# Kernel tuning notes

Measured on AMD Instinct MI355X. Metric: run time of the kernel, lower is better.

## Reference

```python
import math
import jax, jax.numpy as jnp
import numpy as np

PROB_SPARSE_FACTOR = 0.4


def setup_inputs() -> dict:
    key = jax.random.key(0)
    kq, kk, kv = jax.random.split(key, 3)
    B, H, T, S, D = 2, 16, 2048, 2048, 64
    q = jax.random.normal(kq, (B, H, T, D), dtype=jnp.float32)
    k = jax.random.normal(kk, (B, H, S, D), dtype=jnp.float32)
    v = jax.random.normal(kv, (B, H, S, D), dtype=jnp.float32)
    return {"q": q, "k": k, "v": v}


def reference(q, k, v):
    B, H, T, D = q.shape
    S = k.shape[2]
    scaling = 1.0 / math.sqrt(D)
    # Informer-style top-u query count (static, derived from shapes)
    u = max(int(min(PROB_SPARSE_FACTOR * math.log(S), T * 0.5)), int(T * 0.3))

    # KLD scoring over full attention approximation: [B,H,T,S]
    attn_approx = jnp.einsum("bhtd,bhsd->bhts", q * scaling, k)
    attn_approx = jnp.clip(attn_approx, -50.0, 50.0)
    attn_approx = attn_approx - jnp.max(attn_approx, axis=-1, keepdims=True)
    sm = jax.nn.softmax(attn_approx, axis=-1)
    log_uniform = math.log(S)
    kl_score = jnp.sum(sm * (jnp.log(sm + 1e-10) + log_uniform), axis=-1)  # [B,H,T]

    # Select top-u most informative queries per (b,h)
    _, topk_idx = jax.lax.top_k(kl_score, u)  # [B,H,u]

    # Sparse attention only for selected queries
    q_red = jnp.take_along_axis(q, topk_idx[..., None], axis=2)  # [B,H,u,D]
    scores = jnp.einsum("bhud,bhsd->bhus", q_red, k) * scaling
    scores = jnp.clip(scores, -50.0, 50.0)
    scores = scores - jnp.max(scores, axis=-1, keepdims=True)
    w = jax.nn.softmax(scores, axis=-1)
    w = jnp.clip(w, 1e-9, 1.0)
    out_red = jnp.einsum("bhus,bhsd->bhud", w, v)  # [B,H,u,D]

    # Scatter reduced outputs back into a zero-initialized full output
    b_i = jnp.arange(B)[:, None, None]
    h_i = jnp.arange(H)[None, :, None]
    out = jnp.zeros_like(q).at[b_i, h_i, topk_idx].set(out_red)
    return out
```

## Files before the change

### kernel.cpp

```cpp
#include <hip/hip_runtime.h>
#include <math.h>

#define T_DIM 2048
#define S_DIM 2048
#define D_DIM 64
#define BH_DIM 32
#define U_SEL 614
#define LOG_S_D 7.624618986159398
#define LOG2E_F 1.4426950408889634f
#define LN2_D 0.6931471805599453
#define SCL_Q (0.125f * LOG2E_F)

typedef __attribute__((ext_vector_type(8))) short bf16x8;
typedef __attribute__((ext_vector_type(4))) short bf16x4;
typedef __attribute__((ext_vector_type(4))) float f32x4;

__device__ __forceinline__ unsigned short bf16_rne(float x) {
  unsigned u = __float_as_uint(x);
  u += 0x7FFF + ((u >> 16) & 1);
  return (unsigned short)(u >> 16);
}
__device__ __forceinline__ float bf16_to_f(unsigned short h) {
  return __uint_as_float(((unsigned)h) << 16);
}

#define GLD_LDS16(g, l)                                                        \
  __builtin_amdgcn_global_load_lds(                                            \
      (const __attribute__((address_space(1))) unsigned int*)(const void*)(g), \
      (__attribute__((address_space(3))) unsigned int*)(void*)(l), 16, 0, 0)

__device__ __forceinline__ void stage_img16(const unsigned short* __restrict__ g,
                                            unsigned short* l, int lane, int w) {
#pragma unroll
  for (int it = 0; it < 4; ++it) {
    const int chunk = it * 4 + w;
    GLD_LDS16((const char*)g + chunk * 1024 + lane * 16, (char*)l + chunk * 1024);
  }
}
__device__ __forceinline__ void stage_img8(const unsigned short* __restrict__ g,
                                           unsigned short* l, int lane, int w) {
#pragma unroll
  for (int it = 0; it < 2; ++it) {
    const int chunk = it * 4 + w;
    GLD_LDS16((const char*)g + chunk * 1024 + lane * 16, (char*)l + chunk * 1024);
  }
}

__device__ __forceinline__ bf16x8 ldfrag_sw(const unsigned short* buf, int row, int chunk) {
  return *(const bf16x8*)(buf + (row << 6) + (((chunk) ^ (row & 7)) << 3));
}
__device__ __forceinline__ bf16x8 ldfrag_k128(const unsigned short* buf, int row, int chunk) {
  return *(const bf16x8*)(buf + ((row >> 6) << 12) + ((row & 63) << 6) +
                          (((chunk) ^ (row & 7)) << 3));
}

__global__ __launch_bounds__(256) void convert_kernel(
    const float* __restrict__ kin, const float* __restrict__ vin,
    unsigned short* __restrict__ kimg, unsigned short* __restrict__ vt_g,
    float* __restrict__ out) {
  __shared__ float vld[128][65];
  const int jb = blockIdx.x;
  const int tid = threadIdx.x;
  if (jb < 1024) {
    const int bh = jb >> 5, tl = jb & 31;
    const float* src = kin + ((size_t)bh * 2048 + tl * 64) * 64;
    unsigned short* dst = kimg + (size_t)(bh * 32 + tl) * 8192;
#pragma unroll
    for (int g = 0; g < 2; ++g) {
      const int flat = g * 256 + tid;
      const int r = flat >> 3, c = flat & 7;
      const float4 f0 = *(const float4*)(src + r * 64 + c * 8);
      const float4 f1 = *(const float4*)(src + r * 64 + c * 8 + 4);
      const float xs[8] = {f0.x, f0.y, f0.z, f0.w, f1.x, f1.y, f1.z, f1.w};
      bf16x8 hv, lv;
#pragma unroll
      for (int j = 0; j < 8; ++j) {
        const unsigned short h = bf16_rne(xs[j]);
        hv[j] = (short)h;
        lv[j] = (short)bf16_rne(xs[j] - bf16_to_f(h));
      }
      const int base = (r << 6) + ((c ^ (r & 7)) << 3);
      *(bf16x8*)(dst + base) = hv;
      *(bf16x8*)(dst + 4096 + base) = lv;
    }
  } else if (jb < 1536) {
    const int jv = jb - 1024;
    const int bh = jv >> 4, tl = jv & 15;
    const float* src = vin + ((size_t)bh * 2048 + tl * 128) * 64;
#pragma unroll
    for (int g = 0; g < 8; ++g) {
      const int f = g * 256 + tid;
      const int r = f >> 4, c4 = f & 15;
      const float4 x = *(const float4*)(src + r * 64 + c4 * 4);
      vld[r][c4 * 4 + 0] = x.x;
      vld[r][c4 * 4 + 1] = x.y;
      vld[r][c4 * 4 + 2] = x.z;
      vld[r][c4 * 4 + 3] = x.w;
    }
    __syncthreads();
    unsigned short* dst = vt_g + (size_t)(bh * 16 + tl) * 8192;
#pragma unroll
    for (int g = 0; g < 4; ++g) {
      const int oc = g * 256 + tid;
      const int d = oc >> 4, cc = oc & 15;
      bf16x8 hv;
#pragma unroll
      for (int j = 0; j < 8; ++j) hv[j] = (short)bf16_rne(vld[cc * 8 + j][d]);
      *(bf16x8*)(dst + (d << 7) + (((cc ^ (d & 15))) << 3)) = hv;
    }
  } else {
    float4* o4 = (float4*)out;
    const size_t b = (size_t)(jb - 1536);
#pragma unroll
    for (int g = 0; g < 8; ++g)
      o4[b * 2048 + g * 256 + tid] = make_float4(0.f, 0.f, 0.f, 0.f);
  }
}

__global__ __launch_bounds__(256, 4) void kl_score_mfma(
    const float* __restrict__ q, const unsigned short* __restrict__ kimg,
    float2* __restrict__ zw) {
  __shared__ __align__(16) unsigned short lbuf[2][8192];
  const int b = blockIdx.x;
  const int bh = b & 31;
  const int t0 = ((b >> 5) & 15) * 128;
  const int shalf = b >> 9;
  const int tid = threadIdx.x;
  const int lane = tid & 63, w = tid >> 6, quad = lane >> 4, l15 = lane & 15;
  const float* qb = q + (size_t)bh * (2048 * 64) + (size_t)t0 * 64;
  const unsigned short* kb = kimg + (size_t)bh * (32 * 8192);
  const int tg0 = shalf * 16;

  {
#pragma unroll
    for (int g = 0; g < 4; ++g) {
      const int flat = g * 256 + tid;
      const int r = flat >> 3, c = flat & 7;
      const float4 f0 = *(const float4*)(qb + r * 64 + c * 8);
      const float4 f1 = *(const float4*)(qb + r * 64 + c * 8 + 4);
      const float xs[8] = {f0.x, f0.y, f0.z, f0.w, f1.x, f1.y, f1.z, f1.w};
      bf16x8 hv, lv;
#pragma unroll
      for (int j = 0; j < 8; ++j) {
        const float x = xs[j] * SCL_Q;
        const unsigned short h = bf16_rne(x);
        hv[j] = (short)h;
        lv[j] = (short)bf16_rne(x - bf16_to_f(h));
      }
      const int r2 = r & 63, hi2 = r >> 6;
      const int base = hi2 * 4096 + (r2 << 6) + ((c ^ (r2 & 7)) << 3);
      *(bf16x8*)(&lbuf[0][0] + base) = hv;
      *(bf16x8*)(&lbuf[1][0] + base) = lv;
    }
  }
  __syncthreads();

  bf16x8 ah[2][2], al[2][2];
#pragma unroll
  for (int rt = 0; rt < 2; ++rt) {
    const int row = w * 32 + rt * 16 + l15;
#pragma unroll
    for (int kc = 0; kc < 2; ++kc) {
      ah[rt][kc] = ldfrag_k128(&lbuf[0][0], row, kc * 4 + quad);
      al[rt][kc] = ldfrag_k128(&lbuf[1][0], row, kc * 4 + quad);
    }
  }
  __syncthreads();

  stage_img16(kb + (size_t)tg0 * 8192, &lbuf[0][0], lane, w);
  __syncthreads();

  float Zf[8], Wf[8];
#pragma unroll
  for (int i = 0; i < 8; ++i) { Zf[i] = 0.f; Wf[i] = 0.f; }

  for (int t = 0; t < 16; ++t) {
    if (t < 15)
      stage_img16(kb + (size_t)(tg0 + t + 1) * 8192, &lbuf[(t + 1) & 1][0], lane, w);
    const unsigned short* cb = &lbuf[t & 1][0];

    f32x4 acc[2][4];
#pragma unroll
    for (int rt = 0; rt < 2; ++rt)
#pragma unroll
      for (int ct = 0; ct < 4; ++ct) acc[rt][ct] = (f32x4){0.f, 0.f, 0.f, 0.f};

#pragma unroll
    for (int ct = 0; ct < 4; ++ct) {
      const int srow = ct * 16 + l15;
      const bf16x8 bh0 = ldfrag_sw(cb, srow, quad);
      const bf16x8 bl0 = ldfrag_sw(cb + 4096, srow, quad);
      const bf16x8 bh1 = ldfrag_sw(cb, srow, 4 + quad);
      const bf16x8 bl1 = ldfrag_sw(cb + 4096, srow, 4 + quad);
#pragma unroll
      for (int rt = 0; rt < 2; ++rt) {
        f32x4 c = acc[rt][ct];
        c = __builtin_amdgcn_mfma_f32_16x16x32_bf16(ah[rt][0], bh0, c, 0, 0, 0);
        c = __builtin_amdgcn_mfma_f32_16x16x32_bf16(al[rt][0], bh0, c, 0, 0, 0);
        c = __builtin_amdgcn_mfma_f32_16x16x32_bf16(ah[rt][0], bl0, c, 0, 0, 0);
        c = __builtin_amdgcn_mfma_f32_16x16x32_bf16(ah[rt][1], bh1, c, 0, 0, 0);
        c = __builtin_amdgcn_mfma_f32_16x16x32_bf16(al[rt][1], bh1, c, 0, 0, 0);
        c = __builtin_amdgcn_mfma_f32_16x16x32_bf16(ah[rt][1], bl1, c, 0, 0, 0);
        acc[rt][ct] = c;
      }
    }

#pragma unroll
    for (int rt = 0; rt < 2; ++rt)
#pragma unroll
      for (int r = 0; r < 4; ++r) {
        float zp = 0.f, wp = 0.f;
#pragma unroll
        for (int ct = 0; ct < 4; ++ct) {
          const float tt = acc[rt][ct][r];
          const float e = exp2f(tt);
          zp += e;
          wp = fmaf(e, tt, wp);
        }
        Zf[rt * 4 + r] += zp;
        Wf[rt * 4 + r] += wp;
      }
    __syncthreads();
  }

#pragma unroll
  for (int i = 0; i < 8; ++i) {
    float Zt = Zf[i], Wt = Wf[i];
#pragma unroll
    for (int mask = 1; mask <= 8; mask <<= 1) {
      Zt += __shfl_xor(Zt, mask);
      Wt += __shfl_xor(Wt, mask);
    }
    if (l15 == 0) {
      const int row = t0 + w * 32 + (i >> 2) * 16 + quad * 4 + (i & 3);
      zw[((size_t)shalf * 32 + bh) * 2048 + row] = make_float2(Zt, Wt);
    }
  }
}

__global__ __launch_bounds__(1024) void topk_kernel(const float2* __restrict__ zw,
                                                    int* __restrict__ topk) {
  __shared__ float sv[2048];
  __shared__ int si[2048];
  const int bh = blockIdx.x;
  const int tid = threadIdx.x;
  for (int i = tid; i < 2048; i += 1024) {
    const float2 a = zw[(size_t)bh * 2048 + i];
    const float2 c = zw[(size_t)(32 + bh) * 2048 + i];
    const double Z = (double)a.x + (double)c.x;
    const double W = (double)a.y + (double)c.y;
    sv[i] = (float)(LN2_D * (W / Z) - log(Z) + LOG_S_D);
    si[i] = i;
  }
  __syncthreads();
  for (int kk = 2; kk <= 2048; kk <<= 1) {
    for (int j = kk >> 1; j > 0; j >>= 1) {
      const int p = tid;
      const int i = ((p & ~(j - 1)) << 1) | (p & (j - 1));
      const int pr = i | j;
      const float v1 = sv[i], v2 = sv[pr];
      const int i1 = si[i], i2 = si[pr];
      const bool beforePI = (v2 > v1) || (v2 == v1 && i2 < i1);
      const bool dirDesc = ((i & kk) == 0);
      const bool doSwap = dirDesc ? beforePI : !beforePI;
      if (doSwap) { sv[i] = v2; sv[pr] = v1; si[i] = i2; si[pr] = i1; }
      __syncthreads();
    }
  }
  for (int i = tid; i < U_SEL; i += 1024) topk[bh * U_SEL + i] = si[i];
}

struct __align__(16) SmC {
  unsigned short qs[64 * 64];
  unsigned short kt[128 * 64];
  union { unsigned short vt[64 * 128]; float obuf[64 * 64]; } u;
  unsigned short ps[4][64 * 40];
  float zred[4][64];
};

__global__ __launch_bounds__(256, 3) void sparse_attn_mfma(
    const float* __restrict__ q, const unsigned short* __restrict__ kimg,
    const unsigned short* __restrict__ vt_g, const int* __restrict__ topk,
    float* __restrict__ out) {
  __shared__ SmC sm;
  const int b = blockIdx.x;
  const int bh = b & 31;
  const int l0 = (b >> 5) * 64;
  const int tid = threadIdx.x;
  const int lane = tid & 63, w = tid >> 6, quad = lane >> 4, l15 = lane & 15;
  const float* qb = q + (size_t)bh * (2048 * 64);
  const unsigned short* kb = kimg + (size_t)bh * (32 * 8192);
  const unsigned short* vtb = vt_g + (size_t)bh * (16 * 8192);
  const int* tkb = topk + bh * U_SEL;

  {
#pragma unroll
    for (int g = 0; g < 2; ++g) {
      const int ch = g * 256 + tid;
      const int r = ch >> 3, c = ch & 7;
      const int l = l0 + r;
      const int row = (l < U_SEL) ? tkb[l] : tkb[0];
      const float4 f0 = *(const float4*)(qb + (size_t)row * 64 + c * 8);
      const float4 f1 = *(const float4*)(qb + (size_t)row * 64 + c * 8 + 4);
      const float xs[8] = {f0.x, f0.y, f0.z, f0.w, f1.x, f1.y, f1.z, f1.w};
      bf16x8 hv;
#pragma unroll
      for (int j = 0; j < 8; ++j) hv[j] = (short)bf16_rne(xs[j] * SCL_Q);
      *(bf16x8*)&sm.qs[(r << 6) + ((c ^ (r & 7)) << 3)] = hv;
    }
  }
  stage_img8(kb, sm.kt, lane, w);
  stage_img8(kb + 8192, sm.kt + 4096, lane, w);
  stage_img16(vtb, sm.u.vt, lane, w);
  __syncthreads();

  bf16x8 qf[4][2];
#pragma unroll
  for (int nt = 0; nt < 4; ++nt)
#pragma unroll
    for (int kc = 0; kc < 2; ++kc)
      qf[nt][kc] = ldfrag_sw(sm.qs, nt * 16 + l15, kc * 4 + quad);

  float zrun[4] = {0.f, 0.f, 0.f, 0.f};
  f32x4 oacc[4][4];
#pragma unroll
  for (int a = 0; a < 4; ++a)
#pragma unroll
    for (int b2 = 0; b2 < 4; ++b2) oacc[a][b2] = (f32x4){0.f, 0.f, 0.f, 0.f};

  for (int st = 0; st < 16; ++st) {
    f32x4 sacc[2][4];
#pragma unroll
    for (int mt = 0; mt < 2; ++mt)
#pragma unroll
      for (int nt = 0; nt < 4; ++nt) sacc[mt][nt] = (f32x4){0.f, 0.f, 0.f, 0.f};
#pragma unroll
    for (int mt = 0; mt < 2; ++mt) {
      const int arow = w * 32 + mt * 16 + l15;
      const bf16x8 a0 = ldfrag_k128(sm.kt, arow, quad);
      const bf16x8 a1 = ldfrag_k128(sm.kt, arow, 4 + quad);
#pragma unroll
      for (int nt = 0; nt < 4; ++nt) {
        f32x4 c = sacc[mt][nt];
        c = __builtin_amdgcn_mfma_f32_16x16x32_bf16(a0, qf[nt][0], c, 0, 0, 0);
        c = __builtin_amdgcn_mfma_f32_16x16x32_bf16(a1, qf[nt][1], c, 0, 0, 0);
        sacc[mt][nt] = c;
      }
    }

#pragma unroll
    for (int nt = 0; nt < 4; ++nt) {
      float zl = 0.f;
#pragma unroll
      for (int mt = 0; mt < 2; ++mt) {
        bf16x4 pw;
#pragma unroll
        for (int r = 0; r < 4; ++r) {
          const float p = exp2f(sacc[mt][nt][r]);
          zl += p;
          pw[r] = (short)bf16_rne(p);
        }
        *(bf16x4*)&sm.ps[w][(nt * 16 + l15) * 40 + mt * 16 + quad * 4] = pw;
      }
      zrun[nt] += zl;
    }

    {
      bf16x8 vbf[4];
#pragma unroll
      for (int dt = 0; dt < 4; ++dt) {
        const int d = dt * 16 + l15;
        vbf[dt] = *(const bf16x8*)&sm.u.vt[(d << 7) + (((w * 4 + quad) ^ l15) << 3)];
      }
#pragma unroll
      for (int mtq = 0; mtq < 4; ++mtq) {
        const bf16x8 pa = *(const bf16x8*)&sm.ps[w][(mtq * 16 + l15) * 40 + quad * 8];
#pragma unroll
        for (int dt = 0; dt < 4; ++dt)
          oacc[mtq][dt] = __builtin_amdgcn_mfma_f32_16x16x32_bf16(pa, vbf[dt], oacc[mtq][dt], 0, 0, 0);
      }
    }
    __syncthreads();
    if (st < 15) {
      stage_img8(kb + (size_t)(2 * st + 2) * 8192, sm.kt, lane, w);
      stage_img8(kb + (size_t)(2 * st + 3) * 8192, sm.kt + 4096, lane, w);
      stage_img16(vtb + (size_t)(st + 1) * 8192, sm.u.vt, lane, w);
      __syncthreads();
    }
  }

#pragma unroll
  for (int nt = 0; nt < 4; ++nt) {
    float z = zrun[nt];
    z += __shfl_xor(z, 16);
    z += __shfl_xor(z, 32);
    if (quad == 0) sm.zred[w][nt * 16 + l15] = z;
  }
  for (int i = tid; i < 64 * 64; i += 256) sm.u.obuf[i] = 0.f;
  __syncthreads();
#pragma unroll
  for (int mtq = 0; mtq < 4; ++mtq)
#pragma unroll
    for (int r = 0; r < 4; ++r) {
      const int qr = mtq * 16 + quad * 4 + r;
#pragma unroll
      for (int dt = 0; dt < 4; ++dt)
        atomicAdd(&sm.u.obuf[qr * 64 + dt * 16 + l15], oacc[mtq][dt][r]);
    }
  __syncthreads();
  {
    const int qr = tid >> 2, seg = tid & 3;
    const int l = l0 + qr;
    if (l < U_SEL) {
      const float Zt = sm.zred[0][qr] + sm.zred[1][qr] + sm.zred[2][qr] + sm.zred[3][qr];
      const float inv = 1.0f / Zt;
      const int row = tkb[l];
      float* op = &out[((size_t)bh * T_DIM + row) * 64 + seg * 16];
      const float* ob = &sm.u.obuf[qr * 64 + seg * 16];
#pragma unroll
      for (int j = 0; j < 4; ++j) {
        float4 o;
        o.x = ob[j * 4 + 0] * inv;
        o.y = ob[j * 4 + 1] * inv;
        o.z = ob[j * 4 + 2] * inv;
        o.w = ob[j * 4 + 3] * inv;
        *(float4*)&op[j * 4] = o;
      }
    }
  }
}

extern "C" void kernel_launch(void* const* d_in, const int* in_sizes, int n_in,
                              void* d_out, int out_size, void* d_ws, size_t ws_size,
                              hipStream_t stream) {
  const float* q = (const float*)d_in[0];
  const float* k = (const float*)d_in[1];
  const float* v = (const float*)d_in[2];
  float* out = (float*)d_out;
  char* ws = (char*)d_ws;
  float2* zw = (float2*)ws;
  int* topk = (int*)(ws + 1048576);
  unsigned short* kimg = (unsigned short*)(ws + 1310720);
  unsigned short* vt_g = (unsigned short*)(ws + 18087936);

  convert_kernel<<<dim3(2048), dim3(256), 0, stream>>>(k, v, kimg, vt_g, out);
  kl_score_mfma<<<dim3(1024), dim3(256), 0, stream>>>(q, kimg, zw);
  topk_kernel<<<dim3(BH_DIM), dim3(1024), 0, stream>>>(zw, topk);
  sparse_attn_mfma<<<dim3(320), dim3(256), 0, stream>>>(q, kimg, vt_g, topk, out);
}
```

Measured before the change: 250.2 us.

## Double-buffer K tiles and register-prefetch V to overlap loads with MFMA

K tiles now use two shared-memory buffers, and the next step's K is staged into the idle buffer at the start of each iteration. The next V tile is loaded into registers early and written to shared memory after the barrier. The goal is to hide global-memory latency behind the QK and PV MFMA work instead of stalling after each step. The price is more LDS and registers, so launch bounds drop from 3 to 2 blocks per CU, which cuts occupancy.

```diff
diff --git a/kernel.cpp b/kernel.cpp
--- a/kernel.cpp
+++ b/kernel.cpp
@@ -272,13 +272,13 @@
 
 struct __align__(16) SmC {
   unsigned short qs[64 * 64];
-  unsigned short kt[128 * 64];
-  union { unsigned short vt[64 * 128]; float obuf[64 * 64]; } u;
+  union { unsigned short kt[2][128 * 64]; float obuf[64 * 64]; } u;
+  unsigned short vt[64 * 128];
   unsigned short ps[4][64 * 40];
   float zred[4][64];
 };
 
-__global__ __launch_bounds__(256, 3) void sparse_attn_mfma(
+__global__ __launch_bounds__(256, 2) void sparse_attn_mfma(
     const float* __restrict__ q, const unsigned short* __restrict__ kimg,
     const unsigned short* __restrict__ vt_g, const int* __restrict__ topk,
     float* __restrict__ out) {
@@ -309,9 +309,9 @@
       *(bf16x8*)&sm.qs[(r << 6) + ((c ^ (r & 7)) << 3)] = hv;
     }
   }
-  stage_img8(kb, sm.kt, lane, w);
-  stage_img8(kb + 8192, sm.kt + 4096, lane, w);
-  stage_img16(vtb, sm.u.vt, lane, w);
+  stage_img8(kb, sm.u.kt[0], lane, w);
+  stage_img8(kb + 8192, sm.u.kt[0] + 4096, lane, w);
+  stage_img16(vtb, sm.vt, lane, w);
   __syncthreads();
 
   bf16x8 qf[4][2];
@@ -329,6 +329,19 @@
     for (int b2 = 0; b2 < 4; ++b2) oacc[a][b2] = (f32x4){0.f, 0.f, 0.f, 0.f};
 
   for (int st = 0; st < 16; ++st) {
+    uint4 vr0, vr1, vr2, vr3;
+    if (st < 15) {
+      unsigned short* kdst = sm.u.kt[(st + 1) & 1];
+      stage_img8(kb + (size_t)(2 * st + 2) * 8192, kdst, lane, w);
+      stage_img8(kb + (size_t)(2 * st + 3) * 8192, kdst + 4096, lane, w);
+      const char* vsrc = (const char*)(vtb + (size_t)(st + 1) * 8192) + tid * 16;
+      vr0 = *(const uint4*)(vsrc);
+      vr1 = *(const uint4*)(vsrc + 4096);
+      vr2 = *(const uint4*)(vsrc + 8192);
+      vr3 = *(const uint4*)(vsrc + 12288);
+    }
+    const unsigned short* kcur = sm.u.kt[st & 1];
+
     f32x4 sacc[2][4];
 #pragma unroll
     for (int mt = 0; mt < 2; ++mt)
@@ -337,8 +350,8 @@
 #pragma unroll
     for (int mt = 0; mt < 2; ++mt) {
       const int arow = w * 32 + mt * 16 + l15;
-      const bf16x8 a0 = ldfrag_k128(sm.kt, arow, quad);
-      const bf16x8 a1 = ldfrag_k128(sm.kt, arow, 4 + quad);
+      const bf16x8 a0 = ldfrag_k128(kcur, arow, quad);
+      const bf16x8 a1 = ldfrag_k128(kcur, arow, 4 + quad);
 #pragma unroll
       for (int nt = 0; nt < 4; ++nt) {
         f32x4 c = sacc[mt][nt];
@@ -370,7 +383,7 @@
 #pragma unroll
       for (int dt = 0; dt < 4; ++dt) {
         const int d = dt * 16 + l15;
-        vbf[dt] = *(const bf16x8*)&sm.u.vt[(d << 7) + (((w * 4 + quad) ^ l15) << 3)];
+        vbf[dt] = *(const bf16x8*)&sm.vt[(d << 7) + (((w * 4 + quad) ^ l15) << 3)];
       }
 #pragma unroll
       for (int mtq = 0; mtq < 4; ++mtq) {
@@ -382,9 +395,11 @@
     }
     __syncthreads();
     if (st < 15) {
-      stage_img8(kb + (size_t)(2 * st + 2) * 8192, sm.kt, lane, w);
-      stage_img8(kb + (size_t)(2 * st + 3) * 8192, sm.kt + 4096, lane, w);
-      stage_img16(vtb + (size_t)(st + 1) * 8192, sm.u.vt, lane, w);
+      char* vdst = (char*)sm.vt + tid * 16;
+      *(uint4*)(vdst) = vr0;
+      *(uint4*)(vdst + 4096) = vr1;
+      *(uint4*)(vdst + 8192) = vr2;
+      *(uint4*)(vdst + 12288) = vr3;
       __syncthreads();
     }
   }
```

New measurement: 249.6 us. Within noise of the previous version (-0.2%).

## Split sparse attention over key chunks with atomic accumulation and separate normalize pass

Applied to the files above, without the earlier changes.

The sparse attention kernel now splits the key dimension into four chunks, launching four times as many blocks. Each block accumulates its unnormalized partial outputs and row sums into global memory with atomics, and a new normalize kernel divides by the total afterwards. K and V fragments are read straight from global memory rather than staged in LDS. Probabilities are packed with cvt_pk_bf16 and moved between lanes with shuffles instead of an LDS round-trip. This is meant to fill the GPU better, since 320 blocks under-occupy it, at the cost of global atomics, an extra launch, and an extra read-modify-write of the output rows.

```diff
diff --git a/kernel.cpp b/kernel.cpp
--- a/kernel.cpp
+++ b/kernel.cpp
@@ -14,6 +14,7 @@
 typedef __attribute__((ext_vector_type(8))) short bf16x8;
 typedef __attribute__((ext_vector_type(4))) short bf16x4;
 typedef __attribute__((ext_vector_type(4))) float f32x4;
+typedef __attribute__((ext_vector_type(4))) int i32x4;
 
 __device__ __forceinline__ unsigned short bf16_rne(float x) {
   unsigned u = __float_as_uint(x);
@@ -23,6 +24,11 @@
 __device__ __forceinline__ float bf16_to_f(unsigned short h) {
   return __uint_as_float(((unsigned)h) << 16);
 }
+__device__ __forceinline__ int cvt_pk_bf16(float lo, float hi) {
+  int r;
+  asm("v_cvt_pk_bf16_f32 %0, %1, %2" : "=v"(r) : "v"(lo), "v"(hi));
+  return r;
+}
 
 #define GLD_LDS16(g, l)                                                        \
   __builtin_amdgcn_global_load_lds(                                            \
@@ -37,14 +43,6 @@
     GLD_LDS16((const char*)g + chunk * 1024 + lane * 16, (char*)l + chunk * 1024);
   }
 }
-__device__ __forceinline__ void stage_img8(const unsigned short* __restrict__ g,
-                                           unsigned short* l, int lane, int w) {
-#pragma unroll
-  for (int it = 0; it < 2; ++it) {
-    const int chunk = it * 4 + w;
-    GLD_LDS16((const char*)g + chunk * 1024 + lane * 16, (char*)l + chunk * 1024);
-  }
-}
 
 __device__ __forceinline__ bf16x8 ldfrag_sw(const unsigned short* buf, int row, int chunk) {
   return *(const bf16x8*)(buf + (row << 6) + (((chunk) ^ (row & 7)) << 3));
@@ -57,7 +55,7 @@
 __global__ __launch_bounds__(256) void convert_kernel(
     const float* __restrict__ kin, const float* __restrict__ vin,
     unsigned short* __restrict__ kimg, unsigned short* __restrict__ vt_g,
-    float* __restrict__ out) {
+    float* __restrict__ out, float* __restrict__ zacc) {
   __shared__ float vld[128][65];
   const int jb = blockIdx.x;
   const int tid = threadIdx.x;
@@ -108,12 +106,18 @@
       for (int j = 0; j < 8; ++j) hv[j] = (short)bf16_rne(vld[cc * 8 + j][d]);
       *(bf16x8*)(dst + (d << 7) + (((cc ^ (d & 15))) << 3)) = hv;
     }
-  } else {
+  } else if (jb < 2048) {
     float4* o4 = (float4*)out;
     const size_t b = (size_t)(jb - 1536);
 #pragma unroll
     for (int g = 0; g < 8; ++g)
       o4[b * 2048 + g * 256 + tid] = make_float4(0.f, 0.f, 0.f, 0.f);
+  } else {
+    float4* z4 = (float4*)zacc;
+    const size_t b = (size_t)(jb - 2048);
+#pragma unroll
+    for (int g = 0; g < 8; ++g)
+      z4[b * 2048 + g * 256 + tid] = make_float4(0.f, 0.f, 0.f, 0.f);
   }
 }
 
@@ -271,26 +275,25 @@
 }
 
 struct __align__(16) SmC {
-  unsigned short qs[64 * 64];
-  unsigned short kt[128 * 64];
-  union { unsigned short vt[64 * 128]; float obuf[64 * 64]; } u;
-  unsigned short ps[4][64 * 40];
+  union { unsigned short qs[64 * 64]; float obuf[64 * 64]; } u;
   float zred[4][64];
 };
 
 __global__ __launch_bounds__(256, 3) void sparse_attn_mfma(
     const float* __restrict__ q, const unsigned short* __restrict__ kimg,
     const unsigned short* __restrict__ vt_g, const int* __restrict__ topk,
-    float* __restrict__ out) {
+    float* __restrict__ out, float* __restrict__ zacc) {
   __shared__ SmC sm;
   const int b = blockIdx.x;
   const int bh = b & 31;
-  const int l0 = (b >> 5) * 64;
+  const int t = b >> 5;
+  const int schunk = t & 3;
+  const int l0 = (t >> 2) * 64;
   const int tid = threadIdx.x;
   const int lane = tid & 63, w = tid >> 6, quad = lane >> 4, l15 = lane & 15;
   const float* qb = q + (size_t)bh * (2048 * 64);
-  const unsigned short* kb = kimg + (size_t)bh * (32 * 8192);
-  const unsigned short* vtb = vt_g + (size_t)bh * (16 * 8192);
+  const char* kbB = (const char*)(kimg + (size_t)bh * (32 * 8192));
+  const char* vtB = (const char*)(vt_g + (size_t)bh * (16 * 8192));
   const int* tkb = topk + bh * U_SEL;
 
   {
@@ -306,12 +309,9 @@
       bf16x8 hv;
 #pragma unroll
       for (int j = 0; j < 8; ++j) hv[j] = (short)bf16_rne(xs[j] * SCL_Q);
-      *(bf16x8*)&sm.qs[(r << 6) + ((c ^ (r & 7)) << 3)] = hv;
-    }
-  }
-  stage_img8(kb, sm.kt, lane, w);
-  stage_img8(kb + 8192, sm.kt + 4096, lane, w);
-  stage_img16(vtb, sm.u.vt, lane, w);
+      *(bf16x8*)&sm.u.qs[(r << 6) + ((c ^ (r & 7)) << 3)] = hv;
+    }
+  }
   __syncthreads();
 
   bf16x8 qf[4][2];
@@ -319,7 +319,25 @@
   for (int nt = 0; nt < 4; ++nt)
 #pragma unroll
     for (int kc = 0; kc < 2; ++kc)
-      qf[nt][kc] = ldfrag_sw(sm.qs, nt * 16 + l15, kc * 4 + quad);
+      qf[nt][kc] = ldfrag_sw(sm.u.qs, nt * 16 + l15, kc * 4 + quad);
+
+  int kq[2][2];
+#pragma unroll
+  for (int mt = 0; mt < 2; ++mt) {
+    const int base = w * 32 + mt * 16;
+    const int img = base >> 6;
+    const int row64 = (base & 63) + l15;
+    kq[mt][0] = img * 16384 + row64 * 128 + ((quad ^ (l15 & 7)) << 4);
+    kq[mt][1] = img * 16384 + row64 * 128 + (((4 + quad) ^ (l15 & 7)) << 4);
+  }
+  int voff[4];
+#pragma unroll
+  for (int dt = 0; dt < 4; ++dt)
+    voff[dt] = (dt * 16 + l15) * 256 + (((w * 4 + quad) ^ l15) << 4);
+
+  const int sl0 = ((quad & 1) << 5) + l15;
+  const int sl1 = sl0 + 16;
+  const bool hi2 = quad >= 2;
 
   float zrun[4] = {0.f, 0.f, 0.f, 0.f};
   f32x4 oacc[4][4];
@@ -328,66 +346,63 @@
 #pragma unroll
     for (int b2 = 0; b2 < 4; ++b2) oacc[a][b2] = (f32x4){0.f, 0.f, 0.f, 0.f};
 
-  for (int st = 0; st < 16; ++st) {
+  for (int st = 0; st < 4; ++st) {
+    const char* kp = kbB + (size_t)(schunk * 4 + st) * 32768;
+    const char* vp = vtB + (size_t)(schunk * 4 + st) * 16384;
+
+    const bf16x8 a00 = *(const bf16x8*)(kp + kq[0][0]);
+    const bf16x8 a01 = *(const bf16x8*)(kp + kq[0][1]);
+    const bf16x8 a10 = *(const bf16x8*)(kp + kq[1][0]);
+    const bf16x8 a11 = *(const bf16x8*)(kp + kq[1][1]);
+
     f32x4 sacc[2][4];
 #pragma unroll
     for (int mt = 0; mt < 2; ++mt)
 #pragma unroll
-      for (int nt = 0; nt < 4; ++nt) sacc[mt][nt] = (f32x4){0.f, 0.f, 0.f, 0.f};
-#pragma unroll
-    for (int mt = 0; mt < 2; ++mt) {
-      const int arow = w * 32 + mt * 16 + l15;
-      const bf16x8 a0 = ldfrag_k128(sm.kt, arow, quad);
-      const bf16x8 a1 = ldfrag_k128(sm.kt, arow, 4 + quad);
-#pragma unroll
       for (int nt = 0; nt < 4; ++nt) {
-        f32x4 c = sacc[mt][nt];
-        c = __builtin_amdgcn_mfma_f32_16x16x32_bf16(a0, qf[nt][0], c, 0, 0, 0);
-        c = __builtin_amdgcn_mfma_f32_16x16x32_bf16(a1, qf[nt][1], c, 0, 0, 0);
+        f32x4 c = (f32x4){0.f, 0.f, 0.f, 0.f};
+        c = __builtin_amdgcn_mfma_f32_16x16x32_bf16(mt ? a10 : a00, qf[nt][0], c, 0, 0, 0);
+        c = __builtin_amdgcn_mfma_f32_16x16x32_bf16(mt ? a11 : a01, qf[nt][1], c, 0, 0, 0);
         sacc[mt][nt] = c;
       }
-    }
-
+
+    int wd[4][4];
 #pragma unroll
     for (int nt = 0; nt < 4; ++nt) {
-      float zl = 0.f;
-#pragma unroll
-      for (int mt = 0; mt < 2; ++mt) {
-        bf16x4 pw;
-#pragma unroll
-        for (int r = 0; r < 4; ++r) {
-          const float p = exp2f(sacc[mt][nt][r]);
-          zl += p;
-          pw[r] = (short)bf16_rne(p);
-        }
-        *(bf16x4*)&sm.ps[w][(nt * 16 + l15) * 40 + mt * 16 + quad * 4] = pw;
-      }
-      zrun[nt] += zl;
-    }
-
-    {
-      bf16x8 vbf[4];
-#pragma unroll
-      for (int dt = 0; dt < 4; ++dt) {
-        const int d = dt * 16 + l15;
-        vbf[dt] = *(const bf16x8*)&sm.u.vt[(d << 7) + (((w * 4 + quad) ^ l15) << 3)];
-      }
-#pragma unroll
-      for (int mtq = 0; mtq < 4; ++mtq) {
-        const bf16x8 pa = *(const bf16x8*)&sm.ps[w][(mtq * 16 + l15) * 40 + quad * 8];
-#pragma unroll
-        for (int dt = 0; dt < 4; ++dt)
-          oacc[mtq][dt] = __builtin_amdgcn_mfma_f32_16x16x32_bf16(pa, vbf[dt], oacc[mtq][dt], 0, 0, 0);
-      }
-    }
-    __syncthreads();
-    if (st < 15) {
-      stage_img8(kb + (size_t)(2 * st + 2) * 8192, sm.kt, lane, w);
-      stage_img8(kb + (size_t)(2 * st + 3) * 8192, sm.kt + 4096, lane, w);
-      stage_img16(vtb + (size_t)(st + 1) * 8192, sm.u.vt, lane, w);
-      __syncthreads();
-    }
-  }
+      const float p0 = exp2f(sacc[0][nt][0]), p1 = exp2f(sacc[0][nt][1]);
+      const float p2 = exp2f(sacc[0][nt][2]), p3 = exp2f(sacc[0][nt][3]);
+      const float p4 = exp2f(sacc[1][nt][0]), p5 = exp2f(sacc[1][nt][1]);
+      const float p6 = exp2f(sacc[1][nt][2]), p7 = exp2f(sacc[1][nt][3]);
+      zrun[nt] += (p0 + p1 + p2 + p3) + (p4 + p5 + p6 + p7);
+      wd[nt][0] = cvt_pk_bf16(p0, p1);
+      wd[nt][1] = cvt_pk_bf16(p2, p3);
+      wd[nt][2] = cvt_pk_bf16(p4, p5);
+      wd[nt][3] = cvt_pk_bf16(p6, p7);
+    }
+
+    bf16x8 vbf[4];
+#pragma unroll
+    for (int dt = 0; dt < 4; ++dt) vbf[dt] = *(const bf16x8*)(vp + voff[dt]);
+
+#pragma unroll
+    for (int mtq = 0; mtq < 4; ++mtq) {
+      const int a0 = __shfl(wd[mtq][0], sl0), b0 = __shfl(wd[mtq][2], sl0);
+      const int a1 = __shfl(wd[mtq][1], sl0), b1 = __shfl(wd[mtq][3], sl0);
+      const int a2 = __shfl(wd[mtq][0], sl1), b2 = __shfl(wd[mtq][2], sl1);
+      const int a3 = __shfl(wd[mtq][1], sl1), b3 = __shfl(wd[mtq][3], sl1);
+      i32x4 pw;
+      pw[0] = hi2 ? b0 : a0;
+      pw[1] = hi2 ? b1 : a1;
+      pw[2] = hi2 ? b2 : a2;
+      pw[3] = hi2 ? b3 : a3;
+      const bf16x8 pa = __builtin_bit_cast(bf16x8, pw);
+#pragma unroll
+      for (int dt = 0; dt < 4; ++dt)
+        oacc[mtq][dt] = __builtin_amdgcn_mfma_f32_16x16x32_bf16(pa, vbf[dt], oacc[mtq][dt], 0, 0, 0);
+    }
+  }
+
+  __syncthreads();
 
 #pragma unroll
   for (int nt = 0; nt < 4; ++nt) {
@@ -412,21 +427,37 @@
     const int qr = tid >> 2, seg = tid & 3;
     const int l = l0 + qr;
     if (l < U_SEL) {
-      const float Zt = sm.zred[0][qr] + sm.zred[1][qr] + sm.zred[2][qr] + sm.zred[3][qr];
-      const float inv = 1.0f / Zt;
       const int row = tkb[l];
       float* op = &out[((size_t)bh * T_DIM + row) * 64 + seg * 16];
       const float* ob = &sm.u.obuf[qr * 64 + seg * 16];
 #pragma unroll
-      for (int j = 0; j < 4; ++j) {
-        float4 o;
-        o.x = ob[j * 4 + 0] * inv;
-        o.y = ob[j * 4 + 1] * inv;
-        o.z = ob[j * 4 + 2] * inv;
-        o.w = ob[j * 4 + 3] * inv;
-        *(float4*)&op[j * 4] = o;
-      }
-    }
+      for (int j = 0; j < 16; ++j) atomicAdd(&op[j], ob[j]);
+    }
+    if (tid < 64) {
+      const float Zt = sm.zred[0][tid] + sm.zred[1][tid] + sm.zred[2][tid] + sm.zred[3][tid];
+      if (l0 + tid < U_SEL) atomicAdd(&zacc[bh * 640 + l0 + tid], Zt);
+    }
+  }
+}
+
+__global__ __launch_bounds__(256) void normalize_kernel(
+    const int* __restrict__ topk, const float* __restrict__ zacc,
+    float* __restrict__ out) {
+  const int b = blockIdx.x;
+  const int bh = b & 31;
+  const int l0 = (b >> 5) * 64;
+  const int tid = threadIdx.x;
+  const int qr = tid >> 2, seg = tid & 3;
+  const int l = l0 + qr;
+  if (l >= U_SEL) return;
+  const int row = topk[bh * U_SEL + l];
+  const float inv = 1.0f / zacc[bh * 640 + l];
+  float* op = &out[((size_t)bh * T_DIM + row) * 64 + seg * 16];
+#pragma unroll
+  for (int j = 0; j < 4; ++j) {
+    float4 o = *(float4*)&op[j * 4];
+    o.x *= inv; o.y *= inv; o.z *= inv; o.w *= inv;
+    *(float4*)&op[j * 4] = o;
   }
 }
 
@@ -440,11 +471,13 @@
   char* ws = (char*)d_ws;
   float2* zw = (float2*)ws;
   int* topk = (int*)(ws + 1048576);
+  float* zacc = (float*)(ws + 1131520);
   unsigned short* kimg = (unsigned short*)(ws + 1310720);
   unsigned short* vt_g = (unsigned short*)(ws + 18087936);
 
-  convert_kernel<<<dim3(2048), dim3(256), 0, stream>>>(k, v, kimg, vt_g, out);
+  convert_kernel<<<dim3(2051), dim3(256), 0, stream>>>(k, v, kimg, vt_g, out, zacc);
   kl_score_mfma<<<dim3(1024), dim3(256), 0, stream>>>(q, kimg, zw);
   topk_kernel<<<dim3(BH_DIM), dim3(1024), 0, stream>>>(zw, topk);
-  sparse_attn_mfma<<<dim3(320), dim3(256), 0, stream>>>(q, kimg, vt_g, topk, out);
-}
+  sparse_attn_mfma<<<dim3(1280), dim3(256), 0, stream>>>(q, kimg, vt_g, topk, out, zacc);
+  normalize_kernel<<<dim3(320), dim3(256), 0, stream>>>(topk, zacc, out);
+}
```

New measurement: 569.9 us. 128% more time.

## Double-buffer K/V tiles in sparse attention and widen query tile to 80 rows

Applied to the files above, without the earlier changes.

The sparse attention kernel now double-buffers the K and V shared-memory tiles, issuing loads for the next stage before computing on the current one. This removes one barrier per iteration and overlaps staging with MFMA work. The query tile grows from 64 to 80 rows, so 256 blocks cover the 614 selected queries instead of 320, one block per CU. s_setprio is raised around the MFMA sections. Shared memory grows and occupancy drops to one block per CU, so latency hiding relies on the double buffer.

```diff
diff --git a/kernel.cpp b/kernel.cpp
--- a/kernel.cpp
+++ b/kernel.cpp
@@ -6,6 +6,7 @@
 #define D_DIM 64
 #define BH_DIM 32
 #define U_SEL 614
+#define QROWS 80
 #define LOG_S_D 7.624618986159398
 #define LOG2E_F 1.4426950408889634f
 #define LN2_D 0.6931471805599453
@@ -271,21 +272,20 @@
 }
 
 struct __align__(16) SmC {
-  unsigned short qs[64 * 64];
-  unsigned short kt[128 * 64];
-  union { unsigned short vt[64 * 128]; float obuf[64 * 64]; } u;
-  unsigned short ps[4][64 * 40];
-  float zred[4][64];
+  union { unsigned short kt[2][8192]; float obuf[QROWS * 64]; } a;
+  union { unsigned short vt[2][8192]; float zred[4][QROWS]; } b;
+  unsigned short qs[QROWS * 64];
+  unsigned short ps[4][QROWS * 40];
 };
 
-__global__ __launch_bounds__(256, 3) void sparse_attn_mfma(
+__global__ __launch_bounds__(256, 1) void sparse_attn_mfma(
     const float* __restrict__ q, const unsigned short* __restrict__ kimg,
     const unsigned short* __restrict__ vt_g, const int* __restrict__ topk,
     float* __restrict__ out) {
   __shared__ SmC sm;
   const int b = blockIdx.x;
   const int bh = b & 31;
-  const int l0 = (b >> 5) * 64;
+  const int l0 = (b >> 5) * QROWS;
   const int tid = threadIdx.x;
   const int lane = tid & 63, w = tid >> 6, quad = lane >> 4, l15 = lane & 15;
   const float* qb = q + (size_t)bh * (2048 * 64);
@@ -295,61 +295,73 @@
 
   {
 #pragma unroll
-    for (int g = 0; g < 2; ++g) {
+    for (int g = 0; g < 3; ++g) {
       const int ch = g * 256 + tid;
-      const int r = ch >> 3, c = ch & 7;
-      const int l = l0 + r;
-      const int row = (l < U_SEL) ? tkb[l] : tkb[0];
-      const float4 f0 = *(const float4*)(qb + (size_t)row * 64 + c * 8);
-      const float4 f1 = *(const float4*)(qb + (size_t)row * 64 + c * 8 + 4);
-      const float xs[8] = {f0.x, f0.y, f0.z, f0.w, f1.x, f1.y, f1.z, f1.w};
-      bf16x8 hv;
-#pragma unroll
-      for (int j = 0; j < 8; ++j) hv[j] = (short)bf16_rne(xs[j] * SCL_Q);
-      *(bf16x8*)&sm.qs[(r << 6) + ((c ^ (r & 7)) << 3)] = hv;
-    }
-  }
-  stage_img8(kb, sm.kt, lane, w);
-  stage_img8(kb + 8192, sm.kt + 4096, lane, w);
-  stage_img16(vtb, sm.u.vt, lane, w);
-  __syncthreads();
-
-  bf16x8 qf[4][2];
-#pragma unroll
-  for (int nt = 0; nt < 4; ++nt)
+      if (ch < QROWS * 8) {
+        const int r = ch >> 3, c = ch & 7;
+        const int l = l0 + r;
+        const int row = (l < U_SEL) ? tkb[l] : tkb[0];
+        const float4 f0 = *(const float4*)(qb + (size_t)row * 64 + c * 8);
+        const float4 f1 = *(const float4*)(qb + (size_t)row * 64 + c * 8 + 4);
+        const float xs[8] = {f0.x, f0.y, f0.z, f0.w, f1.x, f1.y, f1.z, f1.w};
+        bf16x8 hv;
+#pragma unroll
+        for (int j = 0; j < 8; ++j) hv[j] = (short)bf16_rne(xs[j] * SCL_Q);
+        *(bf16x8*)&sm.qs[(r << 6) + ((c ^ (r & 7)) << 3)] = hv;
+      }
+    }
+  }
+  stage_img8(kb, sm.a.kt[0], lane, w);
+  stage_img8(kb + 8192, sm.a.kt[0] + 4096, lane, w);
+  stage_img16(vtb, sm.b.vt[0], lane, w);
+  __syncthreads();
+
+  bf16x8 qf[5][2];
+#pragma unroll
+  for (int nt = 0; nt < 5; ++nt)
 #pragma unroll
     for (int kc = 0; kc < 2; ++kc)
       qf[nt][kc] = ldfrag_sw(sm.qs, nt * 16 + l15, kc * 4 + quad);
 
-  float zrun[4] = {0.f, 0.f, 0.f, 0.f};
-  f32x4 oacc[4][4];
-#pragma unroll
-  for (int a = 0; a < 4; ++a)
+  float zrun[5] = {0.f, 0.f, 0.f, 0.f, 0.f};
+  f32x4 oacc[5][4];
+#pragma unroll
+  for (int a = 0; a < 5; ++a)
 #pragma unroll
     for (int b2 = 0; b2 < 4; ++b2) oacc[a][b2] = (f32x4){0.f, 0.f, 0.f, 0.f};
 
   for (int st = 0; st < 16; ++st) {
-    f32x4 sacc[2][4];
+    if (st < 15) {
+      unsigned short* kd = sm.a.kt[(st + 1) & 1];
+      unsigned short* vd = sm.b.vt[(st + 1) & 1];
+      stage_img8(kb + (size_t)(2 * st + 2) * 8192, kd, lane, w);
+      stage_img8(kb + (size_t)(2 * st + 3) * 8192, kd + 4096, lane, w);
+      stage_img16(vtb + (size_t)(st + 1) * 8192, vd, lane, w);
+    }
+    const unsigned short* kcur = sm.a.kt[st & 1];
+    const unsigned short* vcur = sm.b.vt[st & 1];
+
+    const int ar0 = w * 32 + l15, ar1 = w * 32 + 16 + l15;
+    const bf16x8 a00 = ldfrag_k128(kcur, ar0, quad);
+    const bf16x8 a01 = ldfrag_k128(kcur, ar0, 4 + quad);
+    const bf16x8 a10 = ldfrag_k128(kcur, ar1, quad);
+    const bf16x8 a11 = ldfrag_k128(kcur, ar1, 4 + quad);
+
+    f32x4 sacc[2][5];
+    __builtin_amdgcn_s_setprio(1);
 #pragma unroll
     for (int mt = 0; mt < 2; ++mt)
 #pragma unroll
-      for (int nt = 0; nt < 4; ++nt) sacc[mt][nt] = (f32x4){0.f, 0.f, 0.f, 0.f};
-#pragma unroll
-    for (int mt = 0; mt < 2; ++mt) {
-      const int arow = w * 32 + mt * 16 + l15;
-      const bf16x8 a0 = ldfrag_k128(sm.kt, arow, quad);
-      const bf16x8 a1 = ldfrag_k128(sm.kt, arow, 4 + quad);
-#pragma unroll
-      for (int nt = 0; nt < 4; ++nt) {
-        f32x4 c = sacc[mt][nt];
-        c = __builtin_amdgcn_mfma_f32_16x16x32_bf16(a0, qf[nt][0], c, 0, 0, 0);
-        c = __builtin_amdgcn_mfma_f32_16x16x32_bf16(a1, qf[nt][1], c, 0, 0, 0);
+      for (int nt = 0; nt < 5; ++nt) {
+        f32x4 c = (f32x4){0.f, 0.f, 0.f, 0.f};
+        c = __builtin_amdgcn_mfma_f32_16x16x32_bf16(mt ? a10 : a00, qf[nt][0], c, 0, 0, 0);
+        c = __builtin_amdgcn_mfma_f32_16x16x32_bf16(mt ? a11 : a01, qf[nt][1], c, 0, 0, 0);
         sacc[mt][nt] = c;
       }
-    }
-
-#pragma unroll
-    for (int nt = 0; nt < 4; ++nt) {
+    __builtin_amdgcn_s_setprio(0);
+
+#pragma unroll
+    for (int nt = 0; nt < 5; ++nt) {
       float zl = 0.f;
 #pragma unroll
       for (int mt = 0; mt < 2; ++mt) {
@@ -365,66 +377,68 @@
       zrun[nt] += zl;
     }
 
-    {
-      bf16x8 vbf[4];
-#pragma unroll
-      for (int dt = 0; dt < 4; ++dt) {
-        const int d = dt * 16 + l15;
-        vbf[dt] = *(const bf16x8*)&sm.u.vt[(d << 7) + (((w * 4 + quad) ^ l15) << 3)];
-      }
-#pragma unroll
-      for (int mtq = 0; mtq < 4; ++mtq) {
-        const bf16x8 pa = *(const bf16x8*)&sm.ps[w][(mtq * 16 + l15) * 40 + quad * 8];
-#pragma unroll
-        for (int dt = 0; dt < 4; ++dt)
-          oacc[mtq][dt] = __builtin_amdgcn_mfma_f32_16x16x32_bf16(pa, vbf[dt], oacc[mtq][dt], 0, 0, 0);
-      }
-    }
+    bf16x8 vbf[4];
+#pragma unroll
+    for (int dt = 0; dt < 4; ++dt) {
+      const int d = dt * 16 + l15;
+      vbf[dt] = *(const bf16x8*)&vcur[(d << 7) + (((w * 4 + quad) ^ l15) << 3)];
+    }
+
+    __builtin_amdgcn_s_setprio(1);
+#pragma unroll
+    for (int mtq = 0; mtq < 5; ++mtq) {
+      const bf16x8 pa = *(const bf16x8*)&sm.ps[w][(mtq * 16 + l15) * 40 + quad * 8];
+#pragma unroll
+      for (int dt = 0; dt < 4; ++dt)
+        oacc[mtq][dt] = __builtin_amdgcn_mfma_f32_16x16x32_bf16(pa, vbf[dt], oacc[mtq][dt], 0, 0, 0);
+    }
+    __builtin_amdgcn_s_setprio(0);
     __syncthreads();
-    if (st < 15) {
-      stage_img8(kb + (size_t)(2 * st + 2) * 8192, sm.kt, lane, w);
-      stage_img8(kb + (size_t)(2 * st + 3) * 8192, sm.kt + 4096, lane, w);
-      stage_img16(vtb + (size_t)(st + 1) * 8192, sm.u.vt, lane, w);
-      __syncthreads();
-    }
-  }
-
-#pragma unroll
-  for (int nt = 0; nt < 4; ++nt) {
+  }
+
+#pragma unroll
+  for (int nt = 0; nt < 5; ++nt) {
     float z = zrun[nt];
     z += __shfl_xor(z, 16);
     z += __shfl_xor(z, 32);
-    if (quad == 0) sm.zred[w][nt * 16 + l15] = z;
-  }
-  for (int i = tid; i < 64 * 64; i += 256) sm.u.obuf[i] = 0.f;
-  __syncthreads();
-#pragma unroll
-  for (int mtq = 0; mtq < 4; ++mtq)
+    if (quad == 0) sm.b.zred[w][nt * 16 + l15] = z;
+  }
+  for (int i = tid; i < QROWS * 64; i += 256) sm.a.obuf[i] = 0.f;
+  __syncthreads();
+#pragma unroll
+  for (int mtq = 0; mtq < 5; ++mtq)
 #pragma unroll
     for (int r = 0; r < 4; ++r) {
       const int qr = mtq * 16 + quad * 4 + r;
 #pragma unroll
       for (int dt = 0; dt < 4; ++dt)
-        atomicAdd(&sm.u.obuf[qr * 64 + dt * 16 + l15], oacc[mtq][dt][r]);
+        atomicAdd(&sm.a.obuf[qr * 64 + dt * 16 + l15], oacc[mtq][dt][r]);
     }
   __syncthreads();
   {
-    const int qr = tid >> 2, seg = tid & 3;
-    const int l = l0 + qr;
-    if (l < U_SEL) {
-      const float Zt = sm.zred[0][qr] + sm.zred[1][qr] + sm.zred[2][qr] + sm.zred[3][qr];
-      const float inv = 1.0f / Zt;
-      const int row = tkb[l];
-      float* op = &out[((size_t)bh * T_DIM + row) * 64 + seg * 16];
-      const float* ob = &sm.u.obuf[qr * 64 + seg * 16];
-#pragma unroll
-      for (int j = 0; j < 4; ++j) {
-        float4 o;
-        o.x = ob[j * 4 + 0] * inv;
-        o.y = ob[j * 4 + 1] * inv;
-        o.z = ob[j * 4 + 2] * inv;
-        o.w = ob[j * 4 + 3] * inv;
-        *(float4*)&op[j * 4] = o;
+#pragma unroll
+    for (int it = 0; it < 2; ++it) {
+      const int tt = it * 256 + tid;
+      if (tt < QROWS * 4) {
+        const int qr = tt >> 2, seg = tt & 3;
+        const int l = l0 + qr;
+        if (l < U_SEL) {
+          const float Zt = sm.b.zred[0][qr] + sm.b.zred[1][qr] +
+                           sm.b.zred[2][qr] + sm.b.zred[3][qr];
+          const float inv = 1.0f / Zt;
+          const int row = tkb[l];
+          float* op = &out[((size_t)bh * T_DIM + row) * 64 + seg * 16];
+          const float* ob = &sm.a.obuf[qr * 64 + seg * 16];
+#pragma unroll
+          for (int j = 0; j < 4; ++j) {
+            float4 o;
+            o.x = ob[j * 4 + 0] * inv;
+            o.y = ob[j * 4 + 1] * inv;
+            o.z = ob[j * 4 + 2] * inv;
+            o.w = ob[j * 4 + 3] * inv;
+            *(float4*)&op[j * 4] = o;
+          }
+        }
       }
     }
   }
@@ -446,5 +460,5 @@
   convert_kernel<<<dim3(2048), dim3(256), 0, stream>>>(k, v, kimg, vt_g, out);
   kl_score_mfma<<<dim3(1024), dim3(256), 0, stream>>>(q, kimg, zw);
   topk_kernel<<<dim3(BH_DIM), dim3(1024), 0, stream>>>(zw, topk);
-  sparse_attn_mfma<<<dim3(320), dim3(256), 0, stream>>>(q, kimg, vt_g, topk, out);
-}
+  sparse_attn_mfma<<<dim3(256), dim3(256), 0, stream>>>(q, kimg, vt_g, topk, out);
+}
```

Result: faster. 231.2 us (-7.6%).
